# Performance work log

Measured on AMD Instinct MI355X. Metric: run time of the kernel, lower is better.

Reference implementation:

```python
import jax, jax.numpy as jnp
import numpy as np

RADIUS = 2
SIGMA_SPATIAL = 2.5
SIGMA_RANGE_FACTOR = 0.5


def setup_inputs() -> dict:
    key = jax.random.key(0)
    k1, k2 = jax.random.split(key)
    source = jax.random.normal(k1, (4, 64, 64, 64), dtype=jnp.float32)
    guidance = jax.random.uniform(k2, (4, 3, 256, 256), dtype=jnp.float32)
    return {"source": source, "guidance": guidance}


def _jbu(source, guidance):
    # source: [B, C, h, w] low-res features; guidance: [B, Cg, H, W] high-res image
    B, C, h, w = source.shape
    _, Cg, H, W = guidance.shape
    s = H // h  # integer upsampling factor
    r = RADIUS

    # per-batch range sigma from guidance std (torch.std is unbiased -> ddof=1)
    sigma_range = SIGMA_RANGE_FACTOR * jnp.std(guidance, axis=(1, 2, 3), ddof=1)  # [B]
    inv_2sr2 = 1.0 / (2.0 * sigma_range * sigma_range)  # [B]
    inv_2ss2 = 1.0 / (2.0 * SIGMA_SPATIAL * SIGMA_SPATIAL)

    # guidance sampled at low-res cell centers: [B, Cg, h, w]
    off = s // 2
    g_low = guidance[:, :, off::s, off::s]

    # low-res center index for every hi-res pixel
    yc = jnp.arange(H) // s  # [H]
    xc = jnp.arange(W) // s  # [W]

    num = jnp.zeros((B, C, H, W), dtype=source.dtype)
    den = jnp.zeros((B, 1, H, W), dtype=source.dtype)

    # fixed small (2r+1)^2 = 25 window taps; unrolled loop, each tap is a
    # clamped gather + fused weight compute + accumulate (no huge intermediates)
    for dy in range(-r, r + 1):
        yi = jnp.clip(yc + dy, 0, h - 1)  # [H]
        for dx in range(-r, r + 1):
            xi = jnp.clip(xc + dx, 0, w - 1)  # [W]
            src_g = source[:, :, yi[:, None], xi[None, :]]  # [B, C, H, W]
            g_g = g_low[:, :, yi[:, None], xi[None, :]]      # [B, Cg, H, W]
            diff2 = jnp.sum((guidance - g_g) ** 2, axis=1)   # [B, H, W]
            w_range = jnp.exp(-diff2 * inv_2sr2[:, None, None])
            w_spatial = np.exp(-(dy * dy + dx * dx) * 1.0) ** 0.0  # placeholder removed below
            w_spatial = jnp.exp(jnp.asarray(-(dy * dy + dx * dx) * inv_2ss2, dtype=source.dtype))
            wgt = (w_spatial * w_range)[:, None]  # [B, 1, H, W]
            num = num + src_g * wgt
            den = den + wgt

    return num / (den + 1e-8)


def reference(source, guidance):
    return _jbu(source, guidance)
```

## Files before the change

kernel.cpp:

```cpp
#include <hip/hip_runtime.h>

#define B_  4
#define C_  64
#define H_  256
#define W_  256
#define h_  64
#define w_  64
#define L2SW2 (-0.46166241f)
#define L2SW1 (-0.11541560f)

__global__ void jbu_stats(const float* __restrict__ g, double* __restrict__ stats) {
    int b     = blockIdx.x >> 6;
    int slice = blockIdx.x & 63;
    const int perBatch = 3 * H_ * W_;
    const int perBlock = perBatch / 64;
    const float* p = g + (size_t)b * perBatch + (size_t)slice * perBlock;
    double s = 0.0, s2 = 0.0;
    for (int i = threadIdx.x; i < perBlock; i += 256) {
        float v = p[i];
        s  += (double)v;
        s2 += (double)v * (double)v;
    }
    for (int off = 32; off > 0; off >>= 1) {
        s  += __shfl_down(s,  off);
        s2 += __shfl_down(s2, off);
    }
    __shared__ double ls[8];
    int wid  = threadIdx.x >> 6;
    int lane = threadIdx.x & 63;
    if (lane == 0) { ls[wid] = s; ls[4 + wid] = s2; }
    __syncthreads();
    if (threadIdx.x == 0) {
        double S  = ls[0] + ls[1] + ls[2] + ls[3];
        double S2 = ls[4] + ls[5] + ls[6] + ls[7];
        atomicAdd(&stats[b],     S);
        atomicAdd(&stats[4 + b], S2);
    }
}

__global__ __launch_bounds__(256)
void jbu_mega(const float* __restrict__ src, const float* __restrict__ guid,
              const double* __restrict__ stats, float* __restrict__ out) {
    __shared__ __align__(16) float sS[5 * 64 * 12];
    __shared__ __align__(16) float sG[5 * 64 * 4];

    int cg = blockIdx.x & 7;
    int y4 = (blockIdx.x >> 3) & 63;
    int b  = blockIdx.x >> 9;
    int tid = threadIdx.x;

    int yi[5];
    #pragma unroll
    for (int d = 0; d < 5; ++d) {
        int u = y4 + d - 2;
        yi[d] = u < 0 ? 0 : (u > h_ - 1 ? h_ - 1 : u);
    }

    #pragma unroll
    for (int it = 0; it < 10; ++it) {
        int k   = tid + it * 256;
        int xx  = k & 63;
        int cr  = k >> 6;
        int row = cr >> 3;
        int cc  = cr & 7;
        sS[(row * 64 + xx) * 12 + cc] =
            src[(((size_t)b * C_ + cg * 8 + cc) * h_ + yi[row]) * w_ + xx];
    }
    {
        int k = tid;
        #pragma unroll
        for (int it = 0; it < 4; ++it) {
            if (k < 960) {
                int xx  = k & 63;
                int cr  = k >> 6;
                int row = cr / 3;
                int c   = cr - row * 3;
                sG[(row * 64 + xx) * 4 + c] =
                    guid[(((size_t)b * 3 + c) * H_ + (yi[row] * 4 + 2)) * W_ + (xx * 4 + 2)];
            }
            k += 256;
        }
    }

    const double n = 3.0 * H_ * W_;
    double S  = stats[b];
    double S2 = stats[4 + b];
    double var = (S2 - S * S / n) / (n - 1.0);
    float invrl2 = (float)(2.0 / var) * 1.44269504f;

    __syncthreads();

    int x  = tid;
    int y0 = y4 * 4;

    float gp[4][3];
    #pragma unroll
    for (int c = 0; c < 3; ++c)
        #pragma unroll
        for (int p = 0; p < 4; ++p)
            gp[p][c] = guid[(((size_t)b * 3 + c) * H_ + (y0 + p)) * W_ + x];

    int xb = x >> 2;
    int xi[5];
    #pragma unroll
    for (int d = 0; d < 5; ++d) {
        int v = xb + d - 2;
        xi[d] = v < 0 ? 0 : (v > w_ - 1 ? w_ - 1 : v);
    }

    const float l2sw[5] = {L2SW2, L2SW1, 0.0f, L2SW1, L2SW2};

    float acc[4][8];
    float den[4];
    #pragma unroll
    for (int p = 0; p < 4; ++p) {
        den[p] = 0.0f;
        #pragma unroll
        for (int c = 0; c < 8; ++c) acc[p][c] = 0.0f;
    }

    #pragma unroll
    for (int dy = 0; dy < 5; ++dy) {
        float l2y = l2sw[dy];
        int   rb  = dy * 64;
        #pragma unroll
        for (int dx = 0; dx < 5; ++dx) {
            int xx = xi[dx];
            float4 gl = *(const float4*)&sG[(rb + xx) * 4];
            float l2xy = l2y + l2sw[dx];
            float wgt[4];
            #pragma unroll
            for (int p = 0; p < 4; ++p) {
                float d0 = gp[p][0] - gl.x;
                float d1 = gp[p][1] - gl.y;
                float d2 = gp[p][2] - gl.z;
                float diff2 = fmaf(d2, d2, fmaf(d1, d1, d0 * d0));
                float wv = __builtin_amdgcn_exp2f(fmaf(diff2, -invrl2, l2xy));
                wgt[p] = wv;
                den[p] += wv;
            }
            const float* sP = &sS[(rb + xx) * 12];
            float4 s0 = *(const float4*)sP;
            float4 s1 = *(const float4*)(sP + 4);
            #pragma unroll
            for (int p = 0; p < 4; ++p) {
                acc[p][0] = fmaf(wgt[p], s0.x, acc[p][0]);
                acc[p][1] = fmaf(wgt[p], s0.y, acc[p][1]);
                acc[p][2] = fmaf(wgt[p], s0.z, acc[p][2]);
                acc[p][3] = fmaf(wgt[p], s0.w, acc[p][3]);
                acc[p][4] = fmaf(wgt[p], s1.x, acc[p][4]);
                acc[p][5] = fmaf(wgt[p], s1.y, acc[p][5]);
                acc[p][6] = fmaf(wgt[p], s1.z, acc[p][6]);
                acc[p][7] = fmaf(wgt[p], s1.w, acc[p][7]);
            }
        }
    }

    float* ob = out + ((size_t)b * C_ + cg * 8) * H_ * W_;
    #pragma unroll
    for (int p = 0; p < 4; ++p) {
        float r = 1.0f / (den[p] + 1e-8f);
        int row = (y0 + p) * W_ + x;
        #pragma unroll
        for (int c = 0; c < 8; ++c) {
            ob[(size_t)c * H_ * W_ + row] = acc[p][c] * r;
        }
    }
}

extern "C" void kernel_launch(void* const* d_in, const int* in_sizes, int n_in,
                              void* d_out, int out_size, void* d_ws, size_t ws_size,
                              hipStream_t stream) {
    const float* src  = (const float*)d_in[0];
    const float* guid = (const float*)d_in[1];
    float* out = (float*)d_out;

    double* stats = (double*)d_ws;

    hipMemsetAsync(d_ws, 0, 64, stream);
    jbu_stats<<<256, 256, 0, stream>>>(guid, stats);
    jbu_mega<<<B_ * 64 * 8, 256, 0, stream>>>(src, guid, stats, out);
}
```

Baseline: 111.3 us.

## Process 16 channels per block and drop atomics/memset in stats reduction

The main kernel now computes 16 output channels per block instead of 8, so the range weights (exp and guidance diff) are computed once for twice as many channels and the grid is halved. The stats kernel reads float4, writes per-block partial sums instead of using atomics, and the main kernel sums the 32 partials itself, which removes the memset launch. In exchange, register pressure rises with 64 accumulators per thread, the shared tile is larger, and the grid has fewer blocks.

```diff
diff --git a/kernel.cpp b/kernel.cpp
--- a/kernel.cpp
+++ b/kernel.cpp
@@ -10,16 +10,15 @@
 #define L2SW1 (-0.11541560f)
 
 __global__ void jbu_stats(const float* __restrict__ g, double* __restrict__ stats) {
-    int b     = blockIdx.x >> 6;
-    int slice = blockIdx.x & 63;
-    const int perBatch = 3 * H_ * W_;
-    const int perBlock = perBatch / 64;
-    const float* p = g + (size_t)b * perBatch + (size_t)slice * perBlock;
+    int b     = blockIdx.x >> 5;
+    int slice = blockIdx.x & 31;
+    const float4* p = (const float4*)(g + (size_t)b * 3 * H_ * W_) + (size_t)slice * 1536;
     double s = 0.0, s2 = 0.0;
-    for (int i = threadIdx.x; i < perBlock; i += 256) {
-        float v = p[i];
-        s  += (double)v;
-        s2 += (double)v * (double)v;
+    for (int i = threadIdx.x; i < 1536; i += 256) {
+        float4 v = p[i];
+        s  += (double)v.x + (double)v.y + (double)v.z + (double)v.w;
+        s2 += (double)v.x * v.x + (double)v.y * v.y
+            + (double)v.z * v.z + (double)v.w * v.w;
     }
     for (int off = 32; off > 0; off >>= 1) {
         s  += __shfl_down(s,  off);
@@ -31,40 +30,33 @@
     if (lane == 0) { ls[wid] = s; ls[4 + wid] = s2; }
     __syncthreads();
     if (threadIdx.x == 0) {
-        double S  = ls[0] + ls[1] + ls[2] + ls[3];
-        double S2 = ls[4] + ls[5] + ls[6] + ls[7];
-        atomicAdd(&stats[b],     S);
-        atomicAdd(&stats[4 + b], S2);
+        stats[blockIdx.x]       = ls[0] + ls[1] + ls[2] + ls[3];
+        stats[128 + blockIdx.x] = ls[4] + ls[5] + ls[6] + ls[7];
     }
 }
 
-__global__ __launch_bounds__(256)
-void jbu_mega(const float* __restrict__ src, const float* __restrict__ guid,
-              const double* __restrict__ stats, float* __restrict__ out) {
-    __shared__ __align__(16) float sS[5 * 64 * 12];
+__global__ __launch_bounds__(256, 4)
+void jbu_mega16(const float* __restrict__ src, const float* __restrict__ guid,
+                const double* __restrict__ stats, float* __restrict__ out) {
+    __shared__ __align__(16) float sS[5 * 64 * 20];
     __shared__ __align__(16) float sG[5 * 64 * 4];
 
-    int cg = blockIdx.x & 7;
-    int y4 = (blockIdx.x >> 3) & 63;
-    int b  = blockIdx.x >> 9;
+    int cg  = blockIdx.x & 3;
+    int y4  = (blockIdx.x >> 2) & 63;
+    int b   = blockIdx.x >> 8;
     int tid = threadIdx.x;
 
-    int yi[5];
+    const float* sb = src + ((size_t)b * C_ + cg * 16) * h_ * w_;
     #pragma unroll
-    for (int d = 0; d < 5; ++d) {
-        int u = y4 + d - 2;
-        yi[d] = u < 0 ? 0 : (u > h_ - 1 ? h_ - 1 : u);
-    }
-
-    #pragma unroll
-    for (int it = 0; it < 10; ++it) {
+    for (int it = 0; it < 20; ++it) {
         int k   = tid + it * 256;
         int xx  = k & 63;
         int cr  = k >> 6;
-        int row = cr >> 3;
-        int cc  = cr & 7;
-        sS[(row * 64 + xx) * 12 + cc] =
-            src[(((size_t)b * C_ + cg * 8 + cc) * h_ + yi[row]) * w_ + xx];
+        int row = cr >> 4;
+        int cc  = cr & 15;
+        int u   = y4 + row - 2;
+        int yy  = u < 0 ? 0 : (u > h_ - 1 ? h_ - 1 : u);
+        sS[(row * 64 + xx) * 20 + cc] = sb[((size_t)cc * h_ + yy) * w_ + xx];
     }
     {
         int k = tid;
@@ -75,16 +67,21 @@
                 int cr  = k >> 6;
                 int row = cr / 3;
                 int c   = cr - row * 3;
+                int u   = y4 + row - 2;
+                int yy  = u < 0 ? 0 : (u > h_ - 1 ? h_ - 1 : u);
                 sG[(row * 64 + xx) * 4 + c] =
-                    guid[(((size_t)b * 3 + c) * H_ + (yi[row] * 4 + 2)) * W_ + (xx * 4 + 2)];
+                    guid[(((size_t)b * 3 + c) * H_ + (yy * 4 + 2)) * W_ + (xx * 4 + 2)];
             }
             k += 256;
         }
     }
 
+    double S = 0.0, S2 = 0.0;
+    for (int i = 0; i < 32; ++i) {
+        S  += stats[b * 32 + i];
+        S2 += stats[128 + b * 32 + i];
+    }
     const double n = 3.0 * H_ * W_;
-    double S  = stats[b];
-    double S2 = stats[4 + b];
     double var = (S2 - S * S / n) / (n - 1.0);
     float invrl2 = (float)(2.0 / var) * 1.44269504f;
 
@@ -110,13 +107,13 @@
 
     const float l2sw[5] = {L2SW2, L2SW1, 0.0f, L2SW1, L2SW2};
 
-    float acc[4][8];
+    float acc[4][16];
     float den[4];
     #pragma unroll
     for (int p = 0; p < 4; ++p) {
         den[p] = 0.0f;
         #pragma unroll
-        for (int c = 0; c < 8; ++c) acc[p][c] = 0.0f;
+        for (int c = 0; c < 16; ++c) acc[p][c] = 0.0f;
     }
 
     #pragma unroll
@@ -139,30 +136,28 @@
                 wgt[p] = wv;
                 den[p] += wv;
             }
-            const float* sP = &sS[(rb + xx) * 12];
-            float4 s0 = *(const float4*)sP;
-            float4 s1 = *(const float4*)(sP + 4);
+            const float* sP = &sS[(rb + xx) * 20];
             #pragma unroll
-            for (int p = 0; p < 4; ++p) {
-                acc[p][0] = fmaf(wgt[p], s0.x, acc[p][0]);
-                acc[p][1] = fmaf(wgt[p], s0.y, acc[p][1]);
-                acc[p][2] = fmaf(wgt[p], s0.z, acc[p][2]);
-                acc[p][3] = fmaf(wgt[p], s0.w, acc[p][3]);
-                acc[p][4] = fmaf(wgt[p], s1.x, acc[p][4]);
-                acc[p][5] = fmaf(wgt[p], s1.y, acc[p][5]);
-                acc[p][6] = fmaf(wgt[p], s1.z, acc[p][6]);
-                acc[p][7] = fmaf(wgt[p], s1.w, acc[p][7]);
+            for (int q = 0; q < 4; ++q) {
+                float4 sv = *(const float4*)(sP + q * 4);
+                #pragma unroll
+                for (int p = 0; p < 4; ++p) {
+                    acc[p][q * 4 + 0] = fmaf(wgt[p], sv.x, acc[p][q * 4 + 0]);
+                    acc[p][q * 4 + 1] = fmaf(wgt[p], sv.y, acc[p][q * 4 + 1]);
+                    acc[p][q * 4 + 2] = fmaf(wgt[p], sv.z, acc[p][q * 4 + 2]);
+                    acc[p][q * 4 + 3] = fmaf(wgt[p], sv.w, acc[p][q * 4 + 3]);
+                }
             }
         }
     }
 
-    float* ob = out + ((size_t)b * C_ + cg * 8) * H_ * W_;
+    float* ob = out + ((size_t)b * C_ + cg * 16) * H_ * W_;
     #pragma unroll
     for (int p = 0; p < 4; ++p) {
         float r = 1.0f / (den[p] + 1e-8f);
         int row = (y0 + p) * W_ + x;
         #pragma unroll
-        for (int c = 0; c < 8; ++c) {
+        for (int c = 0; c < 16; ++c) {
             ob[(size_t)c * H_ * W_ + row] = acc[p][c] * r;
         }
     }
@@ -177,7 +172,6 @@
 
     double* stats = (double*)d_ws;
 
-    hipMemsetAsync(d_ws, 0, 64, stream);
-    jbu_stats<<<256, 256, 0, stream>>>(guid, stats);
-    jbu_mega<<<B_ * 64 * 8, 256, 0, stream>>>(src, guid, stats, out);
+    jbu_stats<<<128, 256, 0, stream>>>(guid, stats);
+    jbu_mega16<<<B_ * 64 * 4, 256, 0, stream>>>(src, guid, stats, out);
 }
```

New measurement: 97.73 us. -12.2%, faster.
